# Optimization experiments

Hardware: AMD Instinct MI355X
Metric: run time of the kernel (lower is better)

The kernel has to match this reference:

```python
import jax, jax.numpy as jnp
import numpy as np
from jax import lax

BLOCK_SIZE = 5
GAMMA = 0.02


def setup_inputs() -> dict:
    key = jax.random.key(0)
    kx, km = jax.random.split(key)
    N, C, H, W = 64, 64, 80, 80
    x = jax.random.normal(kx, (N, C, H, W), dtype=jnp.float32)
    # Bernoulli(gamma) sample, materialized as an int32 0/1 mask (the module's
    # internal randomness, fixed for deterministic reference comparison).
    mask = (jax.random.uniform(km, (N, C, H, W)) < GAMMA).astype(jnp.int32)
    return {"x": x, "mask": mask}


def _dropblock(x, mask, block_size):
    m = mask.astype(x.dtype)  # 0/1 seed mask, shape (N,C,H,W)
    # Original scatters each seed (h,w) into [h, h+bs) x [w, w+bs) (clipped at
    # H,W). Equivalent dense form: block_mask[i,j] = max over m[i-dh, j-dw],
    # dh,dw in [0,bs) -> sliding-window max with top/left padding of bs-1.
    if block_size > 1:
        block_mask = lax.reduce_window(
            m,
            jnp.array(0.0, x.dtype),
            lax.max,
            window_dimensions=(1, 1, block_size, block_size),
            window_strides=(1, 1, 1, 1),
            padding=((0, 0), (0, 0), (block_size - 1, 0), (block_size - 1, 0)),
        )
    else:
        block_mask = m
    inv_blk_mask = 1.0 - block_mask
    countM = jnp.array(m.size, x.dtype)
    count_ones = inv_blk_mask.sum()
    return inv_blk_mask * x * (countM / count_ones)


def reference(x, mask):
    return _dropblock(x, mask, BLOCK_SIZE)
```

## Files before the change

### kernel.cpp

```cpp
#include <hip/hip_runtime.h>

#define DB_H 80
#define DB_W 80
#define DB_PLANE (DB_H * DB_W)
#define DB_NPLANES 4096
#define DB_ROW_WORDS 3
#define DB_PLANE_WORDS (DB_H * DB_ROW_WORDS)
#define DB_TOTAL (DB_PLANE * DB_NPLANES)
#define DB_COUNT_F 26214400.0f
#define DB_CNT_BYTES (DB_NPLANES * 4)
#define PPBLK 2
#define WPB 4

__global__ __launch_bounds__(256) void db_mask_kernel(
    const int* __restrict__ mask,
    unsigned int* __restrict__ bits,
    unsigned int* __restrict__ counts)
{
    __shared__ unsigned long long P[PPBLK][104];
    __shared__ unsigned int RO[PPBLK][DB_PLANE_WORDS];
    __shared__ unsigned int ZP[PPBLK][2];
    const int t = threadIdx.x;
    const int wid = t >> 6, lane = t & 63;
    const int pib = wid >> 1, half = wid & 1;
    const int plane = blockIdx.x * PPBLK + pib;
    const int* mp = mask + plane * DB_PLANE;
    unsigned long long* Pp = P[pib];
    unsigned int* ro = RO[pib];

    #pragma unroll 1
    for (int c = 0; c < 5; ++c) {
        int v[10];
        const int base = half * 50 + c * 10;
        #pragma unroll
        for (int k = 0; k < 10; ++k) v[k] = mp[(base + k) * 64 + lane];
        #pragma unroll
        for (int k = 0; k < 10; ++k) {
            unsigned long long bal = __ballot(v[k] & 1);
            if (lane == 0) Pp[base + k] = bal;
        }
    }
    if (t < 2 * 4) P[t >> 2][100 + (t & 3)] = 0ULL;
    __syncthreads();

    if (lane < 40) {
        const int r = half * 40 + lane;
        const int bitpos = r * DB_W;
        const int q = bitpos >> 6, off = bitpos & 63;
        unsigned long long a, b;
        if (off) {
            a = (Pp[q] >> off) | (Pp[q + 1] << (64 - off));
            b = (Pp[q + 1] >> off) | (Pp[q + 2] << (64 - off));
        } else {
            a = Pp[q]; b = Pp[q + 1];
        }
        b &= 0xFFFFULL;
        unsigned long long ra = a, rb = b;
        #pragma unroll
        for (int s = 1; s <= 4; ++s) {
            ra |= a << s;
            rb |= (b << s) | (a >> (64 - s));
        }
        rb &= 0xFFFFULL;
        ro[r * 3 + 0] = (unsigned int)ra;
        ro[r * 3 + 1] = (unsigned int)(ra >> 32);
        ro[r * 3 + 2] = (unsigned int)rb;
    }
    __syncthreads();

    unsigned int zeros = 0;
    if (lane < 40) {
        const int i = half * 40 + lane;
        const int lo = (i >= 4) ? i - 4 : 0;
        unsigned int c0 = 0, c1 = 0, c2 = 0;
        for (int ii = lo; ii <= i; ++ii) {
            c0 |= ro[ii * 3 + 0];
            c1 |= ro[ii * 3 + 1];
            c2 |= ro[ii * 3 + 2];
        }
        zeros = 80u - __popc(c0) - __popc(c1) - __popc(c2);
        unsigned int* bp = bits + plane * DB_PLANE_WORDS + i * 3;
        bp[0] = c0; bp[1] = c1; bp[2] = c2;
    }
    for (int off = 32; off > 0; off >>= 1)
        zeros += (unsigned int)__shfl_down((int)zeros, off, 64);
    if (lane == 0) ZP[pib][half] = zeros;
    __syncthreads();
    if (lane == 0 && half == 0)
        counts[plane] = ZP[pib][0] + ZP[pib][1];
}

__global__ __launch_bounds__(256) void db_apply_bits(
    const float4* __restrict__ x,
    const unsigned int* __restrict__ bits,
    const unsigned int* __restrict__ counts,
    float4* __restrict__ out)
{
    __shared__ float s_scale;
    __shared__ unsigned int s_part[4];
    {
        const uint4* cp = (const uint4*)counts;
        unsigned int c = 0;
        #pragma unroll
        for (int k = 0; k < 4; ++k) {
            uint4 v = cp[k * 256 + threadIdx.x];
            c += v.x + v.y + v.z + v.w;
        }
        for (int off = 32; off > 0; off >>= 1)
            c += (unsigned int)__shfl_down((int)c, off, 64);
        if ((threadIdx.x & 63) == 0) s_part[threadIdx.x >> 6] = c;
        __syncthreads();
        if (threadIdx.x == 0)
            s_scale = DB_COUNT_F /
                      (float)(s_part[0] + s_part[1] + s_part[2] + s_part[3]);
        __syncthreads();
    }
    const float scale = s_scale;
    const int NG = DB_TOTAL / 4;
    const int stride = gridDim.x * blockDim.x;
    #pragma unroll 2
    for (int g = blockIdx.x * blockDim.x + threadIdx.x; g < NG; g += stride) {
        int e = g * 4;
        int plane = e / DB_PLANE;
        int ep = e - plane * DB_PLANE;
        int i = ep / DB_W;
        int j = ep - i * DB_W;
        unsigned int nib =
            (bits[plane * DB_PLANE_WORDS + i * 3 + (j >> 5)] >> (j & 31)) & 0xFu;
        float4 v = make_float4(0.f, 0.f, 0.f, 0.f);
        if (nib != 0xFu) v = x[g];
        float4 o;
        o.x = (nib & 1u) ? 0.0f : v.x * scale;
        o.y = (nib & 2u) ? 0.0f : v.y * scale;
        o.z = (nib & 4u) ? 0.0f : v.z * scale;
        o.w = (nib & 8u) ? 0.0f : v.w * scale;
        out[g] = o;
    }
}

__global__ __launch_bounds__(256) void db_count_kernel(
    const int* __restrict__ mask,
    unsigned int* __restrict__ counts)
{
    __shared__ unsigned long long P[WPB][104];
    __shared__ unsigned int RO[WPB][DB_PLANE_WORDS];
    const int wid = threadIdx.x >> 6, lane = threadIdx.x & 63;
    const int plane = blockIdx.x * WPB + wid;
    const int* mp = mask + plane * DB_PLANE;
    unsigned long long* Pp = P[wid];
    unsigned int* ro = RO[wid];
    #pragma unroll 1
    for (int c = 0; c < 10; ++c) {
        int v[10];
        #pragma unroll
        for (int k = 0; k < 10; ++k) v[k] = mp[(c * 10 + k) * 64 + lane];
        #pragma unroll
        for (int k = 0; k < 10; ++k) {
            unsigned long long bal = __ballot(v[k] & 1);
            if (lane == 0) Pp[c * 10 + k] = bal;
        }
    }
    if (lane < 4) Pp[100 + lane] = 0ULL;
    __syncthreads();
    for (int r = lane; r < DB_H; r += 64) {
        const int bitpos = r * DB_W;
        const int q = bitpos >> 6, off = bitpos & 63;
        unsigned long long a, b;
        if (off) {
            a = (Pp[q] >> off) | (Pp[q + 1] << (64 - off));
            b = (Pp[q + 1] >> off) | (Pp[q + 2] << (64 - off));
        } else {
            a = Pp[q]; b = Pp[q + 1];
        }
        b &= 0xFFFFULL;
        unsigned long long ra = a, rb = b;
        #pragma unroll
        for (int s = 1; s <= 4; ++s) {
            ra |= a << s;
            rb |= (b << s) | (a >> (64 - s));
        }
        rb &= 0xFFFFULL;
        ro[r * 3 + 0] = (unsigned int)ra;
        ro[r * 3 + 1] = (unsigned int)(ra >> 32);
        ro[r * 3 + 2] = (unsigned int)rb;
    }
    __syncthreads();
    unsigned int zeros = 0;
    for (int i = lane; i < DB_H; i += 64) {
        const int lo = (i >= 4) ? i - 4 : 0;
        unsigned int c0 = 0, c1 = 0, c2 = 0;
        for (int ii = lo; ii <= i; ++ii) {
            c0 |= ro[ii * 3 + 0];
            c1 |= ro[ii * 3 + 1];
            c2 |= ro[ii * 3 + 2];
        }
        zeros += 80u - __popc(c0) - __popc(c1) - __popc(c2);
    }
    for (int off = 32; off > 0; off >>= 1)
        zeros += (unsigned int)__shfl_down((int)zeros, off, 64);
    if (lane == 0) counts[plane] = zeros;
}

__global__ __launch_bounds__(256) void db_apply_recompute(
    const float* __restrict__ x,
    const int* __restrict__ mask,
    const unsigned int* __restrict__ counts,
    float* __restrict__ out)
{
    __shared__ unsigned long long P[WPB][104];
    __shared__ unsigned int RO[WPB][DB_PLANE_WORDS];
    __shared__ unsigned int BM[WPB][DB_PLANE_WORDS];
    __shared__ float s_scale;
    __shared__ unsigned int s_part[4];
    {
        const uint4* cp = (const uint4*)counts;
        unsigned int c = 0;
        #pragma unroll
        for (int k = 0; k < 4; ++k) {
            uint4 v = cp[k * 256 + threadIdx.x];
            c += v.x + v.y + v.z + v.w;
        }
        for (int off = 32; off > 0; off >>= 1)
            c += (unsigned int)__shfl_down((int)c, off, 64);
        if ((threadIdx.x & 63) == 0) s_part[threadIdx.x >> 6] = c;
        __syncthreads();
        if (threadIdx.x == 0)
            s_scale = DB_COUNT_F /
                      (float)(s_part[0] + s_part[1] + s_part[2] + s_part[3]);
        __syncthreads();
    }
    const float scale = s_scale;
    const int wid = threadIdx.x >> 6, lane = threadIdx.x & 63;
    const int plane = blockIdx.x * WPB + wid;
    const int* mp = mask + plane * DB_PLANE;
    unsigned long long* Pp = P[wid];
    unsigned int* ro = RO[wid];
    #pragma unroll 1
    for (int c = 0; c < 10; ++c) {
        int v[10];
        #pragma unroll
        for (int k = 0; k < 10; ++k) v[k] = mp[(c * 10 + k) * 64 + lane];
        #pragma unroll
        for (int k = 0; k < 10; ++k) {
            unsigned long long bal = __ballot(v[k] & 1);
            if (lane == 0) Pp[c * 10 + k] = bal;
        }
    }
    if (lane < 4) Pp[100 + lane] = 0ULL;
    __syncthreads();
    for (int r = lane; r < DB_H; r += 64) {
        const int bitpos = r * DB_W;
        const int q = bitpos >> 6, off = bitpos & 63;
        unsigned long long a, b;
        if (off) {
            a = (Pp[q] >> off) | (Pp[q + 1] << (64 - off));
            b = (Pp[q + 1] >> off) | (Pp[q + 2] << (64 - off));
        } else {
            a = Pp[q]; b = Pp[q + 1];
        }
        b &= 0xFFFFULL;
        unsigned long long ra = a, rb = b;
        #pragma unroll
        for (int s = 1; s <= 4; ++s) {
            ra |= a << s;
            rb |= (b << s) | (a >> (64 - s));
        }
        rb &= 0xFFFFULL;
        ro[r * 3 + 0] = (unsigned int)ra;
        ro[r * 3 + 1] = (unsigned int)(ra >> 32);
        ro[r * 3 + 2] = (unsigned int)rb;
    }
    __syncthreads();
    unsigned int* bmp = BM[wid];
    for (int i = lane; i < DB_H; i += 64) {
        const int lo = (i >= 4) ? i - 4 : 0;
        unsigned int c0 = 0, c1 = 0, c2 = 0;
        for (int ii = lo; ii <= i; ++ii) {
            c0 |= ro[ii * 3 + 0];
            c1 |= ro[ii * 3 + 1];
            c2 |= ro[ii * 3 + 2];
        }
        bmp[i * 3 + 0] = c0; bmp[i * 3 + 1] = c1; bmp[i * 3 + 2] = c2;
    }
    __syncthreads();
    const float* xp = x + plane * DB_PLANE;
    float* op = out + plane * DB_PLANE;
    for (int e = lane; e < DB_PLANE; e += 64) {
        int i = e / DB_W, j = e - i * DB_W;
        unsigned int wb = bmp[i * 3 + (j >> 5)] >> (j & 31);
        op[e] = (wb & 1u) ? 0.0f : xp[e] * scale;
    }
}

extern "C" void kernel_launch(void* const* d_in, const int* in_sizes, int n_in,
                              void* d_out, int out_size, void* d_ws, size_t ws_size,
                              hipStream_t stream) {
    const float* x = (const float*)d_in[0];
    const int* mask = (const int*)d_in[1];
    float* out = (float*)d_out;

    unsigned int* counts = (unsigned int*)d_ws;
    unsigned int* bits = (unsigned int*)((char*)d_ws + DB_CNT_BYTES);
    const size_t bits_bytes = (size_t)DB_NPLANES * DB_PLANE_WORDS * 4;
    const bool use_bits = ws_size >= DB_CNT_BYTES + bits_bytes;

    if (use_bits) {
        db_mask_kernel<<<DB_NPLANES / PPBLK, 256, 0, stream>>>(mask, bits, counts);
        db_apply_bits<<<2048, 256, 0, stream>>>(
            (const float4*)x, bits, counts, (float4*)out);
    } else {
        db_count_kernel<<<DB_NPLANES / WPB, 256, 0, stream>>>(mask, counts);
        db_apply_recompute<<<DB_NPLANES / WPB, 256, 0, stream>>>(
            x, mask, counts, out);
    }
}
```

Measured before the change: 65.11 us.

## Use bit-plane mask layout with int4 loads and uint4 per-row words

The mask kernel now reads the int mask as int4 and ballots each of the four components separately. This builds four interleaved bit-planes, so each row is stored as one uint4 of 20-bit words indexed by float4 group. The apply kernel then fetches one uint4 per row and tests bit l for each float4 component, which removes the division-by-80 and shift arithmetic. The apply kernel also drops the skip-load of x for fully masked groups, so it always reads x. Each mask block now handles four planes, one per wave, with no inter-wave syncs, at the cost of a larger bit buffer (16 bytes per row instead of 12).

```diff
diff --git a/kernel.cpp b/kernel.cpp
--- a/kernel.cpp
+++ b/kernel.cpp
@@ -4,95 +4,95 @@
 #define DB_W 80
 #define DB_PLANE (DB_H * DB_W)
 #define DB_NPLANES 4096
-#define DB_ROW_WORDS 3
-#define DB_PLANE_WORDS (DB_H * DB_ROW_WORDS)
 #define DB_TOTAL (DB_PLANE * DB_NPLANES)
 #define DB_COUNT_F 26214400.0f
 #define DB_CNT_BYTES (DB_NPLANES * 4)
-#define PPBLK 2
+#define DB_BP_UINT4 (DB_NPLANES * DB_H)
 #define WPB 4
 
-__global__ __launch_bounds__(256) void db_mask_kernel(
-    const int* __restrict__ mask,
-    unsigned int* __restrict__ bits,
+__global__ __launch_bounds__(256) void db_mask_bp(
+    const int4* __restrict__ mask4,
+    uint4* __restrict__ bp,
     unsigned int* __restrict__ counts)
 {
-    __shared__ unsigned long long P[PPBLK][104];
-    __shared__ unsigned int RO[PPBLK][DB_PLANE_WORDS];
-    __shared__ unsigned int ZP[PPBLK][2];
-    const int t = threadIdx.x;
-    const int wid = t >> 6, lane = t & 63;
-    const int pib = wid >> 1, half = wid & 1;
-    const int plane = blockIdx.x * PPBLK + pib;
-    const int* mp = mask + plane * DB_PLANE;
-    unsigned long long* Pp = P[pib];
-    unsigned int* ro = RO[pib];
+    __shared__ unsigned long long G[WPB][26 * 4];
+    __shared__ unsigned int RO[WPB][DB_H * 4];
+    const int wid = threadIdx.x >> 6, lane = threadIdx.x & 63;
+    const int plane = blockIdx.x * WPB + wid;
+    const int4* mp = mask4 + plane * (DB_PLANE / 4);
+    unsigned long long* Gp = G[wid];
+    unsigned int* ro = RO[wid];
+
+    if (lane < 4) Gp[25 * 4 + lane] = 0ULL;
 
     #pragma unroll 1
     for (int c = 0; c < 5; ++c) {
-        int v[10];
-        const int base = half * 50 + c * 10;
-        #pragma unroll
-        for (int k = 0; k < 10; ++k) v[k] = mp[(base + k) * 64 + lane];
-        #pragma unroll
-        for (int k = 0; k < 10; ++k) {
-            unsigned long long bal = __ballot(v[k] & 1);
-            if (lane == 0) Pp[base + k] = bal;
-        }
-    }
-    if (t < 2 * 4) P[t >> 2][100 + (t & 3)] = 0ULL;
-    __syncthreads();
-
-    if (lane < 40) {
-        const int r = half * 40 + lane;
-        const int bitpos = r * DB_W;
-        const int q = bitpos >> 6, off = bitpos & 63;
-        unsigned long long a, b;
-        if (off) {
-            a = (Pp[q] >> off) | (Pp[q + 1] << (64 - off));
-            b = (Pp[q + 1] >> off) | (Pp[q + 2] << (64 - off));
-        } else {
-            a = Pp[q]; b = Pp[q + 1];
-        }
-        b &= 0xFFFFULL;
-        unsigned long long ra = a, rb = b;
-        #pragma unroll
-        for (int s = 1; s <= 4; ++s) {
-            ra |= a << s;
-            rb |= (b << s) | (a >> (64 - s));
-        }
-        rb &= 0xFFFFULL;
-        ro[r * 3 + 0] = (unsigned int)ra;
-        ro[r * 3 + 1] = (unsigned int)(ra >> 32);
-        ro[r * 3 + 2] = (unsigned int)rb;
-    }
-    __syncthreads();
+        int4 v[5];
+        #pragma unroll
+        for (int k = 0; k < 5; ++k) v[k] = mp[(c * 5 + k) * 64 + lane];
+        #pragma unroll
+        for (int k = 0; k < 5; ++k) {
+            unsigned long long b0 = __ballot(v[k].x & 1);
+            unsigned long long b1 = __ballot(v[k].y & 1);
+            unsigned long long b2 = __ballot(v[k].z & 1);
+            unsigned long long b3 = __ballot(v[k].w & 1);
+            if (lane < 4) {
+                unsigned long long bw =
+                    (lane == 0) ? b0 : (lane == 1) ? b1 : (lane == 2) ? b2 : b3;
+                Gp[(c * 5 + k) * 4 + lane] = bw;
+            }
+        }
+    }
+
+    #pragma unroll 1
+    for (int rr = 0; rr < 2; ++rr) {
+        const int r = rr * 64 + lane;
+        if (r < DB_H) {
+            const int e0 = r * DB_W;
+            const int g = e0 >> 8;
+            const int l0 = (e0 & 255) >> 2;
+            const unsigned long long* Gw = Gp + g * 4;
+            const bool cross = l0 > 44;
+            const int sh = 64 - l0;
+            unsigned long long s;
+            unsigned p0, p1, p2, p3;
+            s = Gw[0] >> l0; if (cross) s |= Gw[4] << sh; p0 = (unsigned)s & 0xFFFFF;
+            s = Gw[1] >> l0; if (cross) s |= Gw[5] << sh; p1 = (unsigned)s & 0xFFFFF;
+            s = Gw[2] >> l0; if (cross) s |= Gw[6] << sh; p2 = (unsigned)s & 0xFFFFF;
+            s = Gw[3] >> l0; if (cross) s |= Gw[7] << sh; p3 = (unsigned)s & 0xFFFFF;
+            const unsigned q23 = p2 | p3, q123 = p1 | q23, t = p0 | q123;
+            const unsigned a01 = p0 | p1, a012 = a01 | p2;
+            const unsigned r0 = (p0   | (t    << 1)) & 0xFFFFF;
+            const unsigned r1 = (a01  | (q123 << 1)) & 0xFFFFF;
+            const unsigned r2 = (a012 | (q23  << 1)) & 0xFFFFF;
+            const unsigned r3 = (t    | (p3   << 1)) & 0xFFFFF;
+            ((uint4*)ro)[r] = make_uint4(r0, r1, r2, r3);
+        }
+    }
 
     unsigned int zeros = 0;
-    if (lane < 40) {
-        const int i = half * 40 + lane;
-        const int lo = (i >= 4) ? i - 4 : 0;
-        unsigned int c0 = 0, c1 = 0, c2 = 0;
-        for (int ii = lo; ii <= i; ++ii) {
-            c0 |= ro[ii * 3 + 0];
-            c1 |= ro[ii * 3 + 1];
-            c2 |= ro[ii * 3 + 2];
-        }
-        zeros = 80u - __popc(c0) - __popc(c1) - __popc(c2);
-        unsigned int* bp = bits + plane * DB_PLANE_WORDS + i * 3;
-        bp[0] = c0; bp[1] = c1; bp[2] = c2;
+    #pragma unroll 1
+    for (int rr = 0; rr < 2; ++rr) {
+        const int i = rr * 64 + lane;
+        if (i < DB_H) {
+            const int lo = (i >= 4) ? i - 4 : 0;
+            unsigned c0 = 0, c1 = 0, c2 = 0, c3 = 0;
+            for (int ii = lo; ii <= i; ++ii) {
+                const uint4 rv = ((const uint4*)ro)[ii];
+                c0 |= rv.x; c1 |= rv.y; c2 |= rv.z; c3 |= rv.w;
+            }
+            zeros += 80u - __popc(c0) - __popc(c1) - __popc(c2) - __popc(c3);
+            bp[plane * DB_H + i] = make_uint4(c0, c1, c2, c3);
+        }
     }
     for (int off = 32; off > 0; off >>= 1)
         zeros += (unsigned int)__shfl_down((int)zeros, off, 64);
-    if (lane == 0) ZP[pib][half] = zeros;
-    __syncthreads();
-    if (lane == 0 && half == 0)
-        counts[plane] = ZP[pib][0] + ZP[pib][1];
-}
-
-__global__ __launch_bounds__(256) void db_apply_bits(
+    if (lane == 0) counts[plane] = zeros;
+}
+
+__global__ __launch_bounds__(256) void db_apply_bp(
     const float4* __restrict__ x,
-    const unsigned int* __restrict__ bits,
+    const uint4* __restrict__ bp,
     const unsigned int* __restrict__ counts,
     float4* __restrict__ out)
 {
@@ -116,24 +116,21 @@
         __syncthreads();
     }
     const float scale = s_scale;
-    const int NG = DB_TOTAL / 4;
-    const int stride = gridDim.x * blockDim.x;
+    const unsigned NG = DB_TOTAL / 4;
+    const unsigned stride = gridDim.x * blockDim.x;
     #pragma unroll 2
-    for (int g = blockIdx.x * blockDim.x + threadIdx.x; g < NG; g += stride) {
-        int e = g * 4;
-        int plane = e / DB_PLANE;
-        int ep = e - plane * DB_PLANE;
-        int i = ep / DB_W;
-        int j = ep - i * DB_W;
-        unsigned int nib =
-            (bits[plane * DB_PLANE_WORDS + i * 3 + (j >> 5)] >> (j & 31)) & 0xFu;
-        float4 v = make_float4(0.f, 0.f, 0.f, 0.f);
-        if (nib != 0xFu) v = x[g];
+    for (unsigned g = blockIdx.x * blockDim.x + threadIdx.x; g < NG; g += stride) {
+        const unsigned plane = g / 1600u;
+        const unsigned gp = g - plane * 1600u;
+        const unsigned i = gp / 20u;
+        const unsigned l = gp - i * 20u;
+        const uint4 b = bp[plane * DB_H + i];
+        const float4 v = x[g];
         float4 o;
-        o.x = (nib & 1u) ? 0.0f : v.x * scale;
-        o.y = (nib & 2u) ? 0.0f : v.y * scale;
-        o.z = (nib & 4u) ? 0.0f : v.z * scale;
-        o.w = (nib & 8u) ? 0.0f : v.w * scale;
+        o.x = ((b.x >> l) & 1u) ? 0.0f : v.x * scale;
+        o.y = ((b.y >> l) & 1u) ? 0.0f : v.y * scale;
+        o.z = ((b.z >> l) & 1u) ? 0.0f : v.z * scale;
+        o.w = ((b.w >> l) & 1u) ? 0.0f : v.w * scale;
         out[g] = o;
     }
 }
@@ -143,7 +140,7 @@
     unsigned int* __restrict__ counts)
 {
     __shared__ unsigned long long P[WPB][104];
-    __shared__ unsigned int RO[WPB][DB_PLANE_WORDS];
+    __shared__ unsigned int RO[WPB][DB_H * 3];
     const int wid = threadIdx.x >> 6, lane = threadIdx.x & 63;
     const int plane = blockIdx.x * WPB + wid;
     const int* mp = mask + plane * DB_PLANE;
@@ -208,8 +205,8 @@
     float* __restrict__ out)
 {
     __shared__ unsigned long long P[WPB][104];
-    __shared__ unsigned int RO[WPB][DB_PLANE_WORDS];
-    __shared__ unsigned int BM[WPB][DB_PLANE_WORDS];
+    __shared__ unsigned int RO[WPB][DB_H * 3];
+    __shared__ unsigned int BM[WPB][DB_H * 3];
     __shared__ float s_scale;
     __shared__ unsigned int s_part[4];
     {
@@ -300,14 +297,14 @@
     float* out = (float*)d_out;
 
     unsigned int* counts = (unsigned int*)d_ws;
-    unsigned int* bits = (unsigned int*)((char*)d_ws + DB_CNT_BYTES);
-    const size_t bits_bytes = (size_t)DB_NPLANES * DB_PLANE_WORDS * 4;
-    const bool use_bits = ws_size >= DB_CNT_BYTES + bits_bytes;
-
-    if (use_bits) {
-        db_mask_kernel<<<DB_NPLANES / PPBLK, 256, 0, stream>>>(mask, bits, counts);
-        db_apply_bits<<<2048, 256, 0, stream>>>(
-            (const float4*)x, bits, counts, (float4*)out);
+    uint4* bp = (uint4*)((char*)d_ws + DB_CNT_BYTES);
+    const size_t need = DB_CNT_BYTES + (size_t)DB_BP_UINT4 * sizeof(uint4);
+
+    if (ws_size >= need) {
+        db_mask_bp<<<DB_NPLANES / WPB, 256, 0, stream>>>(
+            (const int4*)mask, bp, counts);
+        db_apply_bp<<<2048, 256, 0, stream>>>(
+            (const float4*)x, bp, counts, (float4*)out);
     } else {
         db_count_kernel<<<DB_NPLANES / WPB, 256, 0, stream>>>(mask, counts);
         db_apply_recompute<<<DB_NPLANES / WPB, 256, 0, stream>>>(
```

Result: slower. 68.02 us (+4.5%).
